# Performance work log

Measured on AMD Instinct MI355X. Metric: run time of the kernel, lower is better.

The kernel has to match this reference:

```python
import jax, jax.numpy as jnp
import numpy as np

B, IN, J, K = 1024, 512, 64, 8
CLAMP_MAX = 10.0

def setup_inputs() -> dict:
    key = jax.random.key(0)
    k1, k2 = jax.random.split(key)
    x = jax.random.normal(k1, (B, IN), dtype=jnp.float32)
    T = jax.random.normal(k2, (IN, J, K), dtype=jnp.float32)
    return {"x": x, "T": T}

def reference(x, T):
    # M: [B, J, K]
    M = jnp.einsum('bi,ijk->bjk', x, T)
    # pairwise diff over batch: [B, B, J, K] (matches torch broadcast M1-M2)
    diff = M[None, :, :, :] - M[:, None, :, :]
    sq = jnp.sum(diff * diff, axis=3)          # [B, B, J]
    # safe sqrt (grad 0 at 0, matching torch.norm subgradient on diagonal)
    sq_safe = jnp.where(sq > 0, sq, 1.0)
    norm = jnp.where(sq > 0, jnp.sqrt(sq_safe), 0.0)
    c = jnp.exp(-jnp.minimum(norm, CLAMP_MAX))  # clamp(max=10) then exp(-.)
    feats = jnp.sum(c, axis=1)                  # [B, J]
    return jnp.concatenate([x, feats], axis=1)  # [B, IN + J]
```

## Files before the change

kernel.cpp:

```cpp
#include <hip/hip_runtime.h>

constexpr int NB  = 1024;
constexpr int NIN = 512;
constexpr int NJ  = 64;
constexpr int NK  = 8;
constexpr int NC  = NJ * NK;
constexpr int OUTC = NIN + NJ;
constexpr float EXPN10 = 4.5399929762484854e-05f;
constexpr float FEAT_BASE = 1024.0f * EXPN10;

typedef __bf16 bf16x8 __attribute__((ext_vector_type(8)));
typedef float floatx16 __attribute__((ext_vector_type(16)));

__device__ __forceinline__ unsigned f2bf(float f) {
  unsigned u = __float_as_uint(f);
  u += 0x7FFFu + ((u >> 16) & 1u);
  return u >> 16;
}

__global__ __launch_bounds__(256) void conv_init_kernel(const float* __restrict__ x,
                                                        const float* __restrict__ T,
                                                        uint4* __restrict__ xb,
                                                        ushort* __restrict__ Tt,
                                                        float* __restrict__ out) {
  __shared__ float Ts[64][65];
  const int bid = blockIdx.x;
  const int tid = threadIdx.x;

  if (bid < 256) {
    const int idx = bid * 256 + tid;
    const float4 v0 = ((const float4*)x)[idx * 2];
    const float4 v1 = ((const float4*)x)[idx * 2 + 1];
    uint4 p;
    p.x = f2bf(v0.x) | (f2bf(v0.y) << 16);
    p.y = f2bf(v0.z) | (f2bf(v0.w) << 16);
    p.z = f2bf(v1.x) | (f2bf(v1.y) << 16);
    p.w = f2bf(v1.z) | (f2bf(v1.w) << 16);
    xb[idx] = p;
  } else if (bid < 320) {
    const int t = bid - 256;
    const int i0 = (t & 7) * 64;
    const int c0 = (t >> 3) * 64;

    const int ti4 = (tid >> 4) * 4;
    const int tc  = (tid & 15) * 4;
#pragma unroll
    for (int r = 0; r < 4; ++r) {
      const float4 v = *(const float4*)&T[(i0 + ti4 + r) * NC + c0 + tc];
      Ts[tc + 0][ti4 + r] = v.x;
      Ts[tc + 1][ti4 + r] = v.y;
      Ts[tc + 2][ti4 + r] = v.z;
      Ts[tc + 3][ti4 + r] = v.w;
    }
    __syncthreads();

    const int co = tid >> 2;
    const int io = (tid & 3) * 16;
    unsigned w[8];
#pragma unroll
    for (int q = 0; q < 8; ++q)
      w[q] = f2bf(Ts[co][io + 2 * q]) | (f2bf(Ts[co][io + 2 * q + 1]) << 16);
    uint4* dst = (uint4*)&Tt[(size_t)(c0 + co) * NIN + i0 + io];
    dst[0] = uint4{w[0], w[1], w[2], w[3]};
    dst[1] = uint4{w[4], w[5], w[6], w[7]};
  } else {
    const int idx = (bid - 320) * 256 + tid;
    const int b = idx / OUTC;
    const int c = idx - b * OUTC;
    out[idx] = (c < NIN) ? x[b * NIN + c] : FEAT_BASE;
  }
}

__global__ __launch_bounds__(256) void gemm_kernel(const uint4* __restrict__ xb,
                                                   const uint4* __restrict__ ttb,
                                                   float* __restrict__ Mp) {
  __shared__ __align__(16) __bf16 Xs[64 * 136];
  __shared__ __align__(16) __bf16 Ts[64 * 136];

  const int tid = threadIdx.x;
  const int b0 = blockIdx.x * 64;
  const int c0 = blockIdx.y * 64;

  const int lane = tid & 63;
  const int w    = tid >> 6;
  const int l31  = lane & 31;
  const int half = lane >> 5;
  const int arow = (w & 1) * 32 + l31;
  const int bcol = (w >> 1) * 32 + l31;

  floatx16 acc = {};

  for (int z = 0; z < 4; ++z) {
#pragma unroll
    for (int t = 0; t < 4; ++t) {
      const int u = t * 256 + tid;
      const int row = u >> 4, seg = u & 15;
      *(uint4*)&Xs[row * 136 + seg * 8] = xb[(b0 + row) * 64 + z * 16 + seg];
      *(uint4*)&Ts[row * 136 + seg * 8] = ttb[(c0 + row) * 64 + z * 16 + seg];
    }
    __syncthreads();

#pragma unroll
    for (int s = 0; s < 8; ++s) {
      const bf16x8 af = *(const bf16x8*)&Xs[arow * 136 + s * 16 + half * 8];
      const bf16x8 bf = *(const bf16x8*)&Ts[bcol * 136 + s * 16 + half * 8];
      acc = __builtin_amdgcn_mfma_f32_32x32x16_bf16(af, bf, acc, 0, 0, 0);
    }
    __syncthreads();
  }

#pragma unroll
  for (int reg = 0; reg < 16; ++reg) {
    const int row = (reg & 3) + 8 * (reg >> 2) + 4 * half;
    const int b = b0 + (w & 1) * 32 + row;
    const int c = c0 + (w >> 1) * 32 + l31;
    Mp[((c >> 3) * NB + b) * NK + (c & 7)] = acc[reg];
  }
}

__global__ __launch_bounds__(256) void prep_kernel(const float* __restrict__ Mp,
                                                   uint4* __restrict__ Mb,
                                                   float* __restrict__ na) {
  const int idx = blockIdx.x * 256 + threadIdx.x;
  const float4 m0 = ((const float4*)Mp)[idx * 2];
  const float4 m1 = ((const float4*)Mp)[idx * 2 + 1];
  float s = m0.x * m0.x;
  s = fmaf(m0.y, m0.y, s); s = fmaf(m0.z, m0.z, s); s = fmaf(m0.w, m0.w, s);
  s = fmaf(m1.x, m1.x, s); s = fmaf(m1.y, m1.y, s); s = fmaf(m1.z, m1.z, s);
  s = fmaf(m1.w, m1.w, s);
  na[idx] = s;
  uint4 p;
  p.x = f2bf(m0.x) | (f2bf(m0.y) << 16);
  p.y = f2bf(m0.z) | (f2bf(m0.w) << 16);
  p.z = f2bf(m1.x) | (f2bf(m1.y) << 16);
  p.w = f2bf(m1.z) | (f2bf(m1.w) << 16);
  Mb[idx] = p;
}

__global__ __launch_bounds__(256) void pairwise_kernel(const uint4* __restrict__ Mb,
                                                       const float* __restrict__ na,
                                                       const float* __restrict__ Mp,
                                                       float* __restrict__ out) {
  const int j    = blockIdx.x;
  const int ag   = blockIdx.y;
  const int bh   = blockIdx.z;
  const int tid  = threadIdx.x;
  const int lane = tid & 63;
  const int w    = tid >> 6;
  const int col  = lane & 31;
  const int h    = lane >> 5;
  const int jb   = j * NB;

  __shared__ uint4 Mb_s[513];
  __shared__ float nb_s[512];
  __shared__ float na_s[128];

  const int bbeg = bh * 512;
  Mb_s[tid]       = Mb[jb + bbeg + tid];
  Mb_s[tid + 256] = Mb[jb + bbeg + tid + 256];
  nb_s[tid]       = na[jb + bbeg + tid];
  nb_s[tid + 256] = na[jb + bbeg + tid + 256];
  if (tid == 0) Mb_s[512] = uint4{0u, 0u, 0u, 0u};

  const int a0 = ag * 128 + w * 32;
  if (lane < 32) na_s[w * 32 + lane] = na[jb + a0 + lane];

  uint4 araw = uint4{0u, 0u, 0u, 0u};
  if (lane < 32) araw = Mb[jb + a0 + lane];
  const bf16x8 af = __builtin_bit_cast(bf16x8, araw);

  __syncthreads();

  float c995[16];
#pragma unroll
  for (int reg = 0; reg < 16; ++reg) {
    const int row = (reg & 3) + 8 * (reg >> 2) + 4 * h;
    c995[reg] = 0.995f * na_s[w * 32 + row];
  }

  const floatx16 zero = {};

#pragma unroll 2
  for (int bt = 0; bt < 16; ++bt) {
    const int bidx = bt * 32 + col;
    const uint4 braw = Mb_s[lane < 32 ? bidx : 512];
    const bf16x8 bf = __builtin_bit_cast(bf16x8, braw);
    const floatx16 P = __builtin_amdgcn_mfma_f32_32x32x16_bf16(af, bf, zero, 0, 0, 0);
    const float nb_l = nb_s[bidx];
    const float rhs = 100.0f - 0.995f * nb_l;

    float t = fmaf(-2.0f, P[0], c995[0]);
#pragma unroll
    for (int reg = 1; reg < 16; ++reg)
      t = fminf(t, fmaf(-2.0f, P[reg], c995[reg]));

    if (__any(t < rhs)) {
#pragma unroll
      for (int reg = 0; reg < 16; ++reg) {
        if (fmaf(-2.0f, P[reg], c995[reg]) < rhs) {
          const int row = (reg & 3) + 8 * (reg >> 2) + 4 * h;
          const int a = a0 + row;
          const int b = bbeg + bt * 32 + col;
          float corr;
          if (a == b) {
            corr = 1.0f - EXPN10;
          } else {
            const float4 av0 = ((const float4*)Mp)[(jb + a) * 2];
            const float4 av1 = ((const float4*)Mp)[(jb + a) * 2 + 1];
            const float4 bv0 = ((const float4*)Mp)[(jb + b) * 2];
            const float4 bv1 = ((const float4*)Mp)[(jb + b) * 2 + 1];
            float d = av0.x - bv0.x; float sq = d * d;
            d = av0.y - bv0.y; sq = fmaf(d, d, sq);
            d = av0.z - bv0.z; sq = fmaf(d, d, sq);
            d = av0.w - bv0.w; sq = fmaf(d, d, sq);
            d = av1.x - bv1.x; sq = fmaf(d, d, sq);
            d = av1.y - bv1.y; sq = fmaf(d, d, sq);
            d = av1.z - bv1.z; sq = fmaf(d, d, sq);
            d = av1.w - bv1.w; sq = fmaf(d, d, sq);
            const float nrm = sqrtf(sq);
            corr = (nrm < 10.0f) ? (__expf(-nrm) - EXPN10) : 0.0f;
          }
          if (corr != 0.0f) atomicAdd(&out[a * OUTC + NIN + j], corr);
        }
      }
    }
  }
}

extern "C" void kernel_launch(void* const* d_in, const int* in_sizes, int n_in,
                              void* d_out, int out_size, void* d_ws, size_t ws_size,
                              hipStream_t stream) {
  const float* x = (const float*)d_in[0];
  const float* T = (const float*)d_in[1];
  float* out = (float*)d_out;

  float* Mp  = (float*)d_ws;
  float* na  = Mp + (size_t)NJ * NB * NK;
  uint4* Mb  = (uint4*)(na + (size_t)NJ * NB);
  uint4* xb  = Mb + (size_t)NJ * NB;
  ushort* Tt = (ushort*)(xb + (size_t)NB * NIN / 8);

  conv_init_kernel<<<dim3(2624), 256, 0, stream>>>(x, T, xb, Tt, out);
  gemm_kernel<<<dim3(16, 8), 256, 0, stream>>>(xb, (const uint4*)Tt, Mp);
  prep_kernel<<<dim3(256), 256, 0, stream>>>(Mp, Mb, na);
  pairwise_kernel<<<dim3(NJ, 8, 2), 256, 0, stream>>>(Mb, na, Mp, out);
}
```

Before: 76.23 us.

## Fuse bf16 conversion, output init and prep into GEMM kernel

Merges the separate conversion/init kernel and the prep kernel into the GEMM kernel. The GEMM now loads fp32 x and T directly, converts them to bf16 while staging into shared memory (transposing T on the fly), then stages the accumulator tile in shared memory to write Mp, the norms and the packed bf16 M. Each block also writes its slice of the output init. This removes two launches and the round-trips through the intermediate buffers, at the cost of more fp32 global traffic per GEMM block, scattered 2-byte LDS stores for the T transpose, and only 128 blocks doing the output init.

```diff
diff --git a/kernel.cpp b/kernel.cpp
--- a/kernel.cpp
+++ b/kernel.cpp
@@ -18,64 +18,16 @@
   return u >> 16;
 }
 
-__global__ __launch_bounds__(256) void conv_init_kernel(const float* __restrict__ x,
-                                                        const float* __restrict__ T,
-                                                        uint4* __restrict__ xb,
-                                                        ushort* __restrict__ Tt,
-                                                        float* __restrict__ out) {
-  __shared__ float Ts[64][65];
-  const int bid = blockIdx.x;
-  const int tid = threadIdx.x;
-
-  if (bid < 256) {
-    const int idx = bid * 256 + tid;
-    const float4 v0 = ((const float4*)x)[idx * 2];
-    const float4 v1 = ((const float4*)x)[idx * 2 + 1];
-    uint4 p;
-    p.x = f2bf(v0.x) | (f2bf(v0.y) << 16);
-    p.y = f2bf(v0.z) | (f2bf(v0.w) << 16);
-    p.z = f2bf(v1.x) | (f2bf(v1.y) << 16);
-    p.w = f2bf(v1.z) | (f2bf(v1.w) << 16);
-    xb[idx] = p;
-  } else if (bid < 320) {
-    const int t = bid - 256;
-    const int i0 = (t & 7) * 64;
-    const int c0 = (t >> 3) * 64;
-
-    const int ti4 = (tid >> 4) * 4;
-    const int tc  = (tid & 15) * 4;
-#pragma unroll
-    for (int r = 0; r < 4; ++r) {
-      const float4 v = *(const float4*)&T[(i0 + ti4 + r) * NC + c0 + tc];
-      Ts[tc + 0][ti4 + r] = v.x;
-      Ts[tc + 1][ti4 + r] = v.y;
-      Ts[tc + 2][ti4 + r] = v.z;
-      Ts[tc + 3][ti4 + r] = v.w;
-    }
-    __syncthreads();
-
-    const int co = tid >> 2;
-    const int io = (tid & 3) * 16;
-    unsigned w[8];
-#pragma unroll
-    for (int q = 0; q < 8; ++q)
-      w[q] = f2bf(Ts[co][io + 2 * q]) | (f2bf(Ts[co][io + 2 * q + 1]) << 16);
-    uint4* dst = (uint4*)&Tt[(size_t)(c0 + co) * NIN + i0 + io];
-    dst[0] = uint4{w[0], w[1], w[2], w[3]};
-    dst[1] = uint4{w[4], w[5], w[6], w[7]};
-  } else {
-    const int idx = (bid - 320) * 256 + tid;
-    const int b = idx / OUTC;
-    const int c = idx - b * OUTC;
-    out[idx] = (c < NIN) ? x[b * NIN + c] : FEAT_BASE;
-  }
-}
-
-__global__ __launch_bounds__(256) void gemm_kernel(const uint4* __restrict__ xb,
-                                                   const uint4* __restrict__ ttb,
-                                                   float* __restrict__ Mp) {
-  __shared__ __align__(16) __bf16 Xs[64 * 136];
-  __shared__ __align__(16) __bf16 Ts[64 * 136];
+__global__ __launch_bounds__(256) void gemm_fused_kernel(const float* __restrict__ x,
+                                                         const float* __restrict__ T,
+                                                         float* __restrict__ Mp,
+                                                         uint4* __restrict__ Mb,
+                                                         float* __restrict__ na,
+                                                         float* __restrict__ out) {
+  __shared__ __align__(16) ushort smem_u[2 * 64 * 136];
+  ushort* Xs = smem_u;
+  ushort* Ts = smem_u + 64 * 136;
+  float*  Cs = (float*)smem_u;
 
   const int tid = threadIdx.x;
   const int b0 = blockIdx.x * 64;
@@ -92,11 +44,29 @@
 
   for (int z = 0; z < 4; ++z) {
 #pragma unroll
-    for (int t = 0; t < 4; ++t) {
-      const int u = t * 256 + tid;
+    for (int p = 0; p < 4; ++p) {
+      const int u = p * 256 + tid;
       const int row = u >> 4, seg = u & 15;
-      *(uint4*)&Xs[row * 136 + seg * 8] = xb[(b0 + row) * 64 + z * 16 + seg];
-      *(uint4*)&Ts[row * 136 + seg * 8] = ttb[(c0 + row) * 64 + z * 16 + seg];
+      const float* src = &x[(b0 + row) * NIN + z * 128 + seg * 8];
+      const float4 v0 = *(const float4*)src;
+      const float4 v1 = *(const float4*)(src + 4);
+      uint4 pk;
+      pk.x = f2bf(v0.x) | (f2bf(v0.y) << 16);
+      pk.y = f2bf(v0.z) | (f2bf(v0.w) << 16);
+      pk.z = f2bf(v1.x) | (f2bf(v1.y) << 16);
+      pk.w = f2bf(v1.z) | (f2bf(v1.w) << 16);
+      *(uint4*)&Xs[row * 136 + seg * 8] = pk;
+    }
+#pragma unroll
+    for (int p = 0; p < 8; ++p) {
+      const int u = p * 256 + tid;
+      const int i_loc = u >> 4;
+      const int cg    = u & 15;
+      const float4 v = *(const float4*)&T[(z * 128 + i_loc) * NC + c0 + cg * 4];
+      Ts[(cg * 4 + 0) * 136 + i_loc] = (ushort)f2bf(v.x);
+      Ts[(cg * 4 + 1) * 136 + i_loc] = (ushort)f2bf(v.y);
+      Ts[(cg * 4 + 2) * 136 + i_loc] = (ushort)f2bf(v.z);
+      Ts[(cg * 4 + 3) * 136 + i_loc] = (ushort)f2bf(v.w);
     }
     __syncthreads();
 
@@ -112,29 +82,41 @@
 #pragma unroll
   for (int reg = 0; reg < 16; ++reg) {
     const int row = (reg & 3) + 8 * (reg >> 2) + 4 * half;
-    const int b = b0 + (w & 1) * 32 + row;
-    const int c = c0 + (w >> 1) * 32 + l31;
-    Mp[((c >> 3) * NB + b) * NK + (c & 7)] = acc[reg];
-  }
-}
-
-__global__ __launch_bounds__(256) void prep_kernel(const float* __restrict__ Mp,
-                                                   uint4* __restrict__ Mb,
-                                                   float* __restrict__ na) {
-  const int idx = blockIdx.x * 256 + threadIdx.x;
-  const float4 m0 = ((const float4*)Mp)[idx * 2];
-  const float4 m1 = ((const float4*)Mp)[idx * 2 + 1];
-  float s = m0.x * m0.x;
-  s = fmaf(m0.y, m0.y, s); s = fmaf(m0.z, m0.z, s); s = fmaf(m0.w, m0.w, s);
-  s = fmaf(m1.x, m1.x, s); s = fmaf(m1.y, m1.y, s); s = fmaf(m1.z, m1.z, s);
-  s = fmaf(m1.w, m1.w, s);
-  na[idx] = s;
-  uint4 p;
-  p.x = f2bf(m0.x) | (f2bf(m0.y) << 16);
-  p.y = f2bf(m0.z) | (f2bf(m0.w) << 16);
-  p.z = f2bf(m1.x) | (f2bf(m1.y) << 16);
-  p.w = f2bf(m1.z) | (f2bf(m1.w) << 16);
-  Mb[idx] = p;
+    Cs[((w & 1) * 32 + row) * 68 + (w >> 1) * 32 + l31] = acc[reg];
+  }
+  __syncthreads();
+
+#pragma unroll
+  for (int pass = 0; pass < 2; ++pass) {
+    const int jl = (tid >> 6) + pass * 4;
+    const int b  = tid & 63;
+    const float4 m0 = *(const float4*)&Cs[b * 68 + jl * 8];
+    const float4 m1 = *(const float4*)&Cs[b * 68 + jl * 8 + 4];
+    const int j_g = blockIdx.y * 8 + jl;
+    const int idx = j_g * NB + b0 + b;
+    ((float4*)Mp)[idx * 2]     = m0;
+    ((float4*)Mp)[idx * 2 + 1] = m1;
+    float s = m0.x * m0.x;
+    s = fmaf(m0.y, m0.y, s); s = fmaf(m0.z, m0.z, s); s = fmaf(m0.w, m0.w, s);
+    s = fmaf(m1.x, m1.x, s); s = fmaf(m1.y, m1.y, s); s = fmaf(m1.z, m1.z, s);
+    s = fmaf(m1.w, m1.w, s);
+    na[idx] = s;
+    uint4 pk;
+    pk.x = f2bf(m0.x) | (f2bf(m0.y) << 16);
+    pk.y = f2bf(m0.z) | (f2bf(m0.w) << 16);
+    pk.z = f2bf(m1.x) | (f2bf(m1.y) << 16);
+    pk.w = f2bf(m1.z) | (f2bf(m1.w) << 16);
+    Mb[idx] = pk;
+  }
+
+  const int obase = (blockIdx.y * 16 + blockIdx.x) * 4608;
+#pragma unroll
+  for (int p = 0; p < 18; ++p) {
+    const int idx = obase + p * 256 + tid;
+    const int b = idx / OUTC;
+    const int c = idx - b * OUTC;
+    out[idx] = (c < NIN) ? x[b * NIN + c] : FEAT_BASE;
+  }
 }
 
 __global__ __launch_bounds__(256) void pairwise_kernel(const uint4* __restrict__ Mb,
@@ -234,14 +216,10 @@
   const float* T = (const float*)d_in[1];
   float* out = (float*)d_out;
 
-  float* Mp  = (float*)d_ws;
-  float* na  = Mp + (size_t)NJ * NB * NK;
-  uint4* Mb  = (uint4*)(na + (size_t)NJ * NB);
-  uint4* xb  = Mb + (size_t)NJ * NB;
-  ushort* Tt = (ushort*)(xb + (size_t)NB * NIN / 8);
-
-  conv_init_kernel<<<dim3(2624), 256, 0, stream>>>(x, T, xb, Tt, out);
-  gemm_kernel<<<dim3(16, 8), 256, 0, stream>>>(xb, (const uint4*)Tt, Mp);
-  prep_kernel<<<dim3(256), 256, 0, stream>>>(Mp, Mb, na);
+  float* Mp = (float*)d_ws;
+  float* na = Mp + (size_t)NJ * NB * NK;
+  uint4* Mb = (uint4*)(na + (size_t)NJ * NB);
+
+  gemm_fused_kernel<<<dim3(16, 8), 256, 0, stream>>>(x, T, Mp, Mb, na, out);
   pairwise_kernel<<<dim3(NJ, 8, 2), 256, 0, stream>>>(Mb, na, Mp, out);
 }
```

New measurement: 90.54 us. 1.19x slower.
